# Performance work log

Measured on AMD Instinct MI355X. Metric: run time of the kernel, lower is better.

The kernel has to match this reference:

```python
import jax, jax.numpy as jnp
import numpy as np

DIM = 128
HEADS = 4


def setup_inputs() -> dict:
    key = jax.random.key(0)
    ks = jax.random.split(key, 6)
    B_, N, C = 2048, 49, DIM
    nW = 64
    x = jax.random.normal(ks[0], (B_, N, C), dtype=jnp.float32)
    mask = jax.random.normal(ks[1], (nW, N, N), dtype=jnp.float32)
    qkv_w = jax.random.normal(ks[2], (3 * C, C), dtype=jnp.float32) * 0.02
    qkv_b = jnp.zeros((3 * C,), dtype=jnp.float32)
    proj_w = jax.random.normal(ks[3], (C, C), dtype=jnp.float32) * 0.02
    proj_b = jnp.zeros((C,), dtype=jnp.float32)
    return {"x": x, "mask": mask, "qkv_w": qkv_w, "qkv_b": qkv_b,
            "proj_w": proj_w, "proj_b": proj_b}


def reference(x, mask, qkv_w, qkv_b, proj_w, proj_b):
    B_, N, C = x.shape
    H = HEADS
    Dh = C // H
    scale = Dh ** (-0.5)
    # fused QKV projection: [B_, N, 3C]
    qkv = x @ qkv_w.T + qkv_b
    qkv = qkv.reshape(B_, N, 3, H, Dh).transpose(2, 0, 3, 1, 4)  # [3, B_, H, N, Dh]
    q, k, v = qkv[0] * scale, qkv[1], qkv[2]
    attn = jnp.einsum('bhqd,bhkd->bhqk', q, k)  # [B_, H, N, N]
    nW = mask.shape[0]
    # add per-window additive mask: broadcast over images and heads
    attn = attn.reshape(B_ // nW, nW, H, N, N) + mask[None, :, None, :, :]
    attn = jax.nn.softmax(attn.reshape(B_, H, N, N), axis=-1)
    out = jnp.einsum('bhqk,bhkd->bhqd', attn, v)  # [B_, H, N, Dh]
    out = out.transpose(0, 2, 1, 3).reshape(B_, N, C)
    return out @ proj_w.T + proj_b
```

## Files before the change

kernel.cpp:

```cpp
#include <hip/hip_runtime.h>

typedef __bf16 bf16_t;
typedef __bf16 bf16x2 __attribute__((ext_vector_type(2)));
typedef __bf16 bf16x4 __attribute__((ext_vector_type(4)));
typedef __bf16 bf16x8 __attribute__((ext_vector_type(8)));
typedef float  f32x4  __attribute__((ext_vector_type(4)));
typedef float  f32x4u __attribute__((ext_vector_type(4), aligned(4)));
typedef short  s16x4  __attribute__((ext_vector_type(4)));
typedef unsigned int u32;

#define MFMA32(a, b, c) __builtin_amdgcn_mfma_f32_16x16x32_bf16((a), (b), (c), 0, 0, 0)

union B4u { bf16x4 h; s16x4 s; };
__device__ __forceinline__ f32x4 MFMA16(bf16x4 a, bf16x4 b, f32x4 c) {
#if __has_builtin(__builtin_amdgcn_mfma_f32_16x16x16_bf16)
    return __builtin_amdgcn_mfma_f32_16x16x16_bf16(a, b, c, 0, 0, 0);
#elif __has_builtin(__builtin_amdgcn_mfma_f32_16x16x16bf16_1k)
    B4u ua, ub; ua.h = a; ub.h = b;
    return __builtin_amdgcn_mfma_f32_16x16x16bf16_1k(ua.s, ub.s, c, 0, 0, 0);
#else
    f32x4 d = c;
    asm volatile("v_mfma_f32_16x16x16_bf16 %0, %1, %2, %0"
                 : "+v"(d) : "v"(a), "v"(b));
    return d;
#endif
}

#define ROWB 272

__device__ __forceinline__ void st4(char* base, int row, int byteoff, bf16x4 v) {
    *(bf16x4*)(base + row * ROWB + byteoff) = v;
}
__device__ __forceinline__ bf16x8 ld8(const char* base, int row, int byteoff) {
    return *(const bf16x8*)(base + row * ROWB + byteoff);
}
__device__ __forceinline__ void stx(char* buf, int i, float4 f) {
    bf16x4 hq;
    hq[0] = (bf16_t)f.x; hq[1] = (bf16_t)f.y; hq[2] = (bf16_t)f.z; hq[3] = (bf16_t)f.w;
    st4(buf, i >> 5, (i & 31) << 3, hq);
}

__device__ __forceinline__ bf16x4 cvt4b(f32x4 v, float4 bias, float sc) {
    bf16x4 t;
    t[0] = (bf16_t)((v[0] + bias.x) * sc);
    t[1] = (bf16_t)((v[1] + bias.y) * sc);
    t[2] = (bf16_t)((v[2] + bias.z) * sc);
    t[3] = (bf16_t)((v[3] + bias.w) * sc);
    return t;
}
__device__ __forceinline__ bf16x4 cvt4s(f32x4 v, float bias) {
    bf16x4 t;
    t[0] = (bf16_t)(v[0] + bias);
    t[1] = (bf16_t)(v[1] + bias);
    t[2] = (bf16_t)(v[2] + bias);
    t[3] = (bf16_t)(v[3] + bias);
    return t;
}

__global__ void wconv_kernel(const float* __restrict__ qw, const float* __restrict__ pw,
                             bf16_t* __restrict__ o) {
    int i = (blockIdx.x * 256 + threadIdx.x) * 4;
    const float* src = (i < 49152) ? (qw + i) : (pw + (i - 49152));
    float4 f = *(const float4*)src;
    bf16x4 h;
    h[0] = (bf16_t)f.x; h[1] = (bf16_t)f.y; h[2] = (bf16_t)f.z; h[3] = (bf16_t)f.w;
    *(bf16x4*)(o + i) = h;
}

template<int USEB>
__device__ __forceinline__ bf16x8 ldw(const float* __restrict__ wf,
                                      const bf16_t* __restrict__ wb, int idx) {
    if constexpr (USEB) {
        return *(const bf16x8*)(wb + idx);
    } else {
        float4 f0 = *(const float4*)(wf + idx);
        float4 f1 = *(const float4*)(wf + idx + 4);
        bf16x8 r;
        r[0] = (bf16_t)f0.x; r[1] = (bf16_t)f0.y; r[2] = (bf16_t)f0.z; r[3] = (bf16_t)f0.w;
        r[4] = (bf16_t)f1.x; r[5] = (bf16_t)f1.y; r[6] = (bf16_t)f1.z; r[7] = (bf16_t)f1.w;
        return r;
    }
}


template<int USEB>
__global__ __launch_bounds__(256, 2) void winattn_kernel(
    const float* __restrict__ xg, const float* __restrict__ maskg,
    const float* __restrict__ qwg, const float* __restrict__ qbg,
    const float* __restrict__ pwg, const float* __restrict__ pbg,
    const bf16_t* __restrict__ wqb, const bf16_t* __restrict__ wpb,
    const int nW, float* __restrict__ outg)
{
    __shared__ char xs[17408];

    const int b    = blockIdx.x;
    const int tid  = threadIdx.x;
    const int w    = tid >> 6;
    const int lane = tid & 63;
    const int g    = lane >> 4;
    const int c0   = lane & 15;
    const int h    = w;

    {
        const float4* xb = (const float4*)(xg + (long)b * 6272);
        #pragma unroll
        for (int it = 0; it < 7; ++it) {
            int i = tid + it * 256;
            if (i < 1568) { float4 f = xb[i]; stx(xs, i, f); }
        }
        #pragma unroll
        for (int it = 0; it < 4; ++it) {
            int i = tid + it * 256;
            if (i < 960) {
                int row = 49 + (i >> 6), byteo = (i & 63) << 2;
                *(u32*)(xs + row * ROWB + byteo) = 0u;
            }
        }
    }
    __syncthreads();

    const float qs = 0.17677669529663687f;

    bf16x4 qfr[2][4];
    {
        f32x4 acc[2][4];
        #pragma unroll
        for (int d = 0; d < 2; ++d)
            #pragma unroll
            for (int mt = 0; mt < 4; ++mt) acc[d][mt] = {0.f, 0.f, 0.f, 0.f};
        #pragma unroll
        for (int ks = 0; ks < 4; ++ks) {
            bf16x8 w0 = ldw<USEB>(qwg, wqb, (32*h + c0) * 128 + 32*ks + 8*g);
            bf16x8 w1 = ldw<USEB>(qwg, wqb, (32*h + 16 + c0) * 128 + 32*ks + 8*g);
            #pragma unroll
            for (int mt = 0; mt < 4; ++mt) {
                bf16x8 xf = ld8(xs, 16*mt + c0, (32*ks + 8*g) * 2);
                acc[0][mt] = MFMA32(w0, xf, acc[0][mt]);
                acc[1][mt] = MFMA32(w1, xf, acc[1][mt]);
            }
        }
        float4 b0 = *(const float4*)(qbg + 32*h + 4*g);
        float4 b1 = *(const float4*)(qbg + 32*h + 16 + 4*g);
        #pragma unroll
        for (int qt = 0; qt < 4; ++qt) {
            qfr[0][qt] = cvt4b(acc[0][qt], b0, qs);
            qfr[1][qt] = cvt4b(acc[1][qt], b1, qs);
        }
    }

    bf16x4 kfr[4][2];
    {
        f32x4 acc[2][4];
        #pragma unroll
        for (int d = 0; d < 2; ++d)
            #pragma unroll
            for (int mt = 0; mt < 4; ++mt) acc[d][mt] = {0.f, 0.f, 0.f, 0.f};
        #pragma unroll
        for (int ks = 0; ks < 4; ++ks) {
            bf16x8 w0 = ldw<USEB>(qwg, wqb, (128 + 32*h + c0) * 128 + 32*ks + 8*g);
            bf16x8 w1 = ldw<USEB>(qwg, wqb, (128 + 32*h + 16 + c0) * 128 + 32*ks + 8*g);
            #pragma unroll
            for (int mt = 0; mt < 4; ++mt) {
                bf16x8 xf = ld8(xs, 16*mt + c0, (32*ks + 8*g) * 2);
                acc[0][mt] = MFMA32(w0, xf, acc[0][mt]);
                acc[1][mt] = MFMA32(w1, xf, acc[1][mt]);
            }
        }
        float4 b0 = *(const float4*)(qbg + 128 + 32*h + 4*g);
        float4 b1 = *(const float4*)(qbg + 128 + 32*h + 16 + 4*g);
        #pragma unroll
        for (int kt = 0; kt < 4; ++kt) {
            kfr[kt][0] = cvt4b(acc[0][kt], b0, 1.f);
            kfr[kt][1] = cvt4b(acc[1][kt], b1, 1.f);
        }
    }

    bf16x4 vfr[2][4];
    {
        f32x4 acc[4][2];
        #pragma unroll
        for (int mt = 0; mt < 4; ++mt)
            #pragma unroll
            for (int d = 0; d < 2; ++d) acc[mt][d] = {0.f, 0.f, 0.f, 0.f};
        #pragma unroll
        for (int ks = 0; ks < 4; ++ks) {
            bf16x8 w0 = ldw<USEB>(qwg, wqb, (256 + 32*h + c0) * 128 + 32*ks + 8*g);
            bf16x8 w1 = ldw<USEB>(qwg, wqb, (256 + 32*h + 16 + c0) * 128 + 32*ks + 8*g);
            #pragma unroll
            for (int mt = 0; mt < 4; ++mt) {
                bf16x8 xf = ld8(xs, 16*mt + c0, (32*ks + 8*g) * 2);
                acc[mt][0] = MFMA32(xf, w0, acc[mt][0]);
                acc[mt][1] = MFMA32(xf, w1, acc[mt][1]);
            }
        }
        float vb0 = qbg[256 + 32*h + c0];
        float vb1 = qbg[256 + 32*h + 16 + c0];
        #pragma unroll
        for (int kt = 0; kt < 4; ++kt) {
            vfr[0][kt] = cvt4s(acc[kt][0], vb0);
            vfr[1][kt] = cvt4s(acc[kt][1], vb1);
        }
    }
    __syncthreads();

    const float* mrow = maskg + (long)(b % nW) * 2401;
    #pragma unroll
    for (int qt = 0; qt < 4; ++qt) {
        f32x4 s[4];
        #pragma unroll
        for (int kt = 0; kt < 4; ++kt) s[kt] = {0.f, 0.f, 0.f, 0.f};
        #pragma unroll
        for (int kt = 0; kt < 4; ++kt) {
            s[kt] = MFMA16(kfr[kt][0], qfr[0][qt], s[kt]);
            s[kt] = MFMA16(kfr[kt][1], qfr[1][qt], s[kt]);
        }

        {
            int q  = 16*qt + c0;
            int qm = q < 49 ? q : 48;
            const float* mr = mrow + qm * 49;
            f32x4u m0 = *(const f32x4u*)(mr + 4*g);
            f32x4u m1 = *(const f32x4u*)(mr + 16 + 4*g);
            f32x4u m2 = *(const f32x4u*)(mr + 32 + 4*g);
            float m48 = mr[48];
            #pragma unroll
            for (int r = 0; r < 4; ++r) {
                s[0][r] += m0[r]; s[1][r] += m1[r]; s[2][r] += m2[r];
            }
            s[3][0] = (g == 0) ? s[3][0] + m48 : -1e30f;
            s[3][1] = -1e30f; s[3][2] = -1e30f; s[3][3] = -1e30f;
        }

        float mx = -1e30f;
        #pragma unroll
        for (int kt = 0; kt < 4; ++kt)
            #pragma unroll
            for (int r = 0; r < 4; ++r) mx = fmaxf(mx, s[kt][r]);
        mx = fmaxf(mx, __shfl_xor(mx, 16));
        mx = fmaxf(mx, __shfl_xor(mx, 32));

        float sum = 0.f;
        bf16x4 p[4];
        #pragma unroll
        for (int kt = 0; kt < 4; ++kt) {
            float e0 = __expf(s[kt][0] - mx), e1 = __expf(s[kt][1] - mx);
            float e2 = __expf(s[kt][2] - mx), e3 = __expf(s[kt][3] - mx);
            sum += (e0 + e1) + (e2 + e3);
            bf16x4 pk;
            pk[0] = (bf16_t)e0; pk[1] = (bf16_t)e1;
            pk[2] = (bf16_t)e2; pk[3] = (bf16_t)e3;
            p[kt] = pk;
        }
        sum += __shfl_xor(sum, 16);
        sum += __shfl_xor(sum, 32);
        float inv = 1.f / sum;

        f32x4 oo[2];
        oo[0] = {0.f, 0.f, 0.f, 0.f}; oo[1] = {0.f, 0.f, 0.f, 0.f};
        #pragma unroll
        for (int kt = 0; kt < 4; ++kt) {
            oo[0] = MFMA16(vfr[0][kt], p[kt], oo[0]);
            oo[1] = MFMA16(vfr[1][kt], p[kt], oo[1]);
        }
        int q = 16*qt + c0;
        #pragma unroll
        for (int dt = 0; dt < 2; ++dt) {
            bf16x4 t;
            t[0] = (bf16_t)(oo[dt][0] * inv); t[1] = (bf16_t)(oo[dt][1] * inv);
            t[2] = (bf16_t)(oo[dt][2] * inv); t[3] = (bf16_t)(oo[dt][3] * inv);
            st4(xs, q, (32*h + 16*dt + 4*g) * 2, t);
        }
    }

    bf16x8 pwf[4][2];
    #pragma unroll
    for (int ks = 0; ks < 4; ++ks) {
        pwf[ks][0] = ldw<USEB>(pwg, wpb, (32*w + c0) * 128 + 32*ks + 8*g);
        pwf[ks][1] = ldw<USEB>(pwg, wpb, (32*w + 16 + c0) * 128 + 32*ks + 8*g);
    }
    float4 pb0 = *(const float4*)(pbg + 32*w + 4*g);
    float4 pb1 = *(const float4*)(pbg + 32*w + 16 + 4*g);
    __syncthreads();

    {
        f32x4 acc[2][4];
        #pragma unroll
        for (int nt = 0; nt < 2; ++nt)
            #pragma unroll
            for (int mt = 0; mt < 4; ++mt) acc[nt][mt] = {0.f, 0.f, 0.f, 0.f};
        #pragma unroll
        for (int ks = 0; ks < 4; ++ks) {
            #pragma unroll
            for (int mt = 0; mt < 4; ++mt) {
                bf16x8 af = ld8(xs, 16*mt + c0, (32*ks + 8*g) * 2);
                acc[0][mt] = MFMA32(pwf[ks][0], af, acc[0][mt]);
                acc[1][mt] = MFMA32(pwf[ks][1], af, acc[1][mt]);
            }
        }
        float* ob = outg + (long)b * 6272;
        #pragma unroll
        for (int nt = 0; nt < 2; ++nt) {
            float4 pb = nt ? pb1 : pb0;
            #pragma unroll
            for (int mt = 0; mt < 4; ++mt) {
                int tok = 16*mt + c0;
                if (tok < 49) {
                    float4 t;
                    t.x = acc[nt][mt][0] + pb.x;
                    t.y = acc[nt][mt][1] + pb.y;
                    t.z = acc[nt][mt][2] + pb.z;
                    t.w = acc[nt][mt][3] + pb.w;
                    *(float4*)(ob + tok*128 + 32*w + 16*nt + 4*g) = t;
                }
            }
        }
    }
}

extern "C" void kernel_launch(void* const* d_in, const int* in_sizes, int n_in,
                              void* d_out, int out_size, void* d_ws, size_t ws_size,
                              hipStream_t stream) {
    const float* xg  = (const float*)d_in[0];
    const float* mg  = (const float*)d_in[1];
    const float* qwg = (const float*)d_in[2];
    const float* qbg = (const float*)d_in[3];
    const float* pwg = (const float*)d_in[4];
    const float* pbg = (const float*)d_in[5];
    float* outg = (float*)d_out;

    const int B  = in_sizes[0] / (49 * 128);
    const int nW = in_sizes[1] / (49 * 49);

    if (d_ws != nullptr && ws_size >= 131072) {
        bf16_t* wqb = (bf16_t*)d_ws;
        bf16_t* wpb = wqb + 49152;
        wconv_kernel<<<64, 256, 0, stream>>>(qwg, pwg, wqb);
        winattn_kernel<1><<<B, 256, 0, stream>>>(
            xg, mg, qwg, qbg, pwg, pbg, wqb, wpb, nW, outg);
    } else {
        winattn_kernel<0><<<B, 256, 0, stream>>>(
            xg, mg, qwg, qbg, pwg, pbg, nullptr, nullptr, nW, outg);
    }
}
```

Measured before the change: 64.92 us.

## Process two windows per 512-thread block with separate LDS tiles

Each block now handles two windows, using 8 waves split into two groups of four heads, each group with its own shared-memory tile. The grid halves and the block size doubles, with an active guard for an odd window count. The aim is to amortise block launch and scheduling overhead and change occupancy, at the cost of both windows sharing the same barriers and possible register-pressure changes under launch_bounds(512,2).

```diff
diff --git a/kernel.cpp b/kernel.cpp
--- a/kernel.cpp
+++ b/kernel.cpp
@@ -27,6 +27,7 @@
 }
 
 #define ROWB 272
+#define TILEB 17408
 
 __device__ __forceinline__ void st4(char* base, int row, int byteoff, bf16x4 v) {
     *(bf16x4*)(base + row * ROWB + byteoff) = v;
@@ -84,33 +85,38 @@
 
 
 template<int USEB>
-__global__ __launch_bounds__(256, 2) void winattn_kernel(
+__global__ __launch_bounds__(512, 2) void winattn_kernel(
     const float* __restrict__ xg, const float* __restrict__ maskg,
     const float* __restrict__ qwg, const float* __restrict__ qbg,
     const float* __restrict__ pwg, const float* __restrict__ pbg,
     const bf16_t* __restrict__ wqb, const bf16_t* __restrict__ wpb,
-    const int nW, float* __restrict__ outg)
+    const int nW, const int Btot, float* __restrict__ outg)
 {
-    __shared__ char xs[17408];
-
-    const int b    = blockIdx.x;
+    __shared__ char xs2[2 * TILEB];
+
     const int tid  = threadIdx.x;
-    const int w    = tid >> 6;
+    const int w8   = tid >> 6;
+    const int win  = w8 >> 2;
+    const int h    = w8 & 3;
     const int lane = tid & 63;
     const int g    = lane >> 4;
     const int c0   = lane & 15;
-    const int h    = w;
-
-    {
-        const float4* xb = (const float4*)(xg + (long)b * 6272);
+
+    const long b     = (long)blockIdx.x * 2 + win;
+    const bool active = (b < Btot);
+    char* xs = xs2 + win * TILEB;
+    const int tid2 = tid & 255;
+
+    if (active) {
+        const float4* xb = (const float4*)(xg + b * 6272);
         #pragma unroll
         for (int it = 0; it < 7; ++it) {
-            int i = tid + it * 256;
+            int i = tid2 + it * 256;
             if (i < 1568) { float4 f = xb[i]; stx(xs, i, f); }
         }
         #pragma unroll
         for (int it = 0; it < 4; ++it) {
-            int i = tid + it * 256;
+            int i = tid2 + it * 256;
             if (i < 960) {
                 int row = 49 + (i >> 6), byteo = (i & 63) << 2;
                 *(u32*)(xs + row * ROWB + byteo) = 0u;
@@ -122,167 +128,173 @@
     const float qs = 0.17677669529663687f;
 
     bf16x4 qfr[2][4];
-    {
-        f32x4 acc[2][4];
-        #pragma unroll
-        for (int d = 0; d < 2; ++d)
-            #pragma unroll
-            for (int mt = 0; mt < 4; ++mt) acc[d][mt] = {0.f, 0.f, 0.f, 0.f};
+    bf16x4 kfr[4][2];
+    bf16x4 vfr[2][4];
+
+    if (active) {
+        {
+            f32x4 acc[2][4];
+            #pragma unroll
+            for (int d = 0; d < 2; ++d)
+                #pragma unroll
+                for (int mt = 0; mt < 4; ++mt) acc[d][mt] = {0.f, 0.f, 0.f, 0.f};
+            #pragma unroll
+            for (int ks = 0; ks < 4; ++ks) {
+                bf16x8 w0 = ldw<USEB>(qwg, wqb, (32*h + c0) * 128 + 32*ks + 8*g);
+                bf16x8 w1 = ldw<USEB>(qwg, wqb, (32*h + 16 + c0) * 128 + 32*ks + 8*g);
+                #pragma unroll
+                for (int mt = 0; mt < 4; ++mt) {
+                    bf16x8 xf = ld8(xs, 16*mt + c0, (32*ks + 8*g) * 2);
+                    acc[0][mt] = MFMA32(w0, xf, acc[0][mt]);
+                    acc[1][mt] = MFMA32(w1, xf, acc[1][mt]);
+                }
+            }
+            float4 b0 = *(const float4*)(qbg + 32*h + 4*g);
+            float4 b1 = *(const float4*)(qbg + 32*h + 16 + 4*g);
+            #pragma unroll
+            for (int qt = 0; qt < 4; ++qt) {
+                qfr[0][qt] = cvt4b(acc[0][qt], b0, qs);
+                qfr[1][qt] = cvt4b(acc[1][qt], b1, qs);
+            }
+        }
+        {
+            f32x4 acc[2][4];
+            #pragma unroll
+            for (int d = 0; d < 2; ++d)
+                #pragma unroll
+                for (int mt = 0; mt < 4; ++mt) acc[d][mt] = {0.f, 0.f, 0.f, 0.f};
+            #pragma unroll
+            for (int ks = 0; ks < 4; ++ks) {
+                bf16x8 w0 = ldw<USEB>(qwg, wqb, (128 + 32*h + c0) * 128 + 32*ks + 8*g);
+                bf16x8 w1 = ldw<USEB>(qwg, wqb, (128 + 32*h + 16 + c0) * 128 + 32*ks + 8*g);
+                #pragma unroll
+                for (int mt = 0; mt < 4; ++mt) {
+                    bf16x8 xf = ld8(xs, 16*mt + c0, (32*ks + 8*g) * 2);
+                    acc[0][mt] = MFMA32(w0, xf, acc[0][mt]);
+                    acc[1][mt] = MFMA32(w1, xf, acc[1][mt]);
+                }
+            }
+            float4 b0 = *(const float4*)(qbg + 128 + 32*h + 4*g);
+            float4 b1 = *(const float4*)(qbg + 128 + 32*h + 16 + 4*g);
+            #pragma unroll
+            for (int kt = 0; kt < 4; ++kt) {
+                kfr[kt][0] = cvt4b(acc[0][kt], b0, 1.f);
+                kfr[kt][1] = cvt4b(acc[1][kt], b1, 1.f);
+            }
+        }
+        {
+            f32x4 acc[4][2];
+            #pragma unroll
+            for (int mt = 0; mt < 4; ++mt)
+                #pragma unroll
+                for (int d = 0; d < 2; ++d) acc[mt][d] = {0.f, 0.f, 0.f, 0.f};
+            #pragma unroll
+            for (int ks = 0; ks < 4; ++ks) {
+                bf16x8 w0 = ldw<USEB>(qwg, wqb, (256 + 32*h + c0) * 128 + 32*ks + 8*g);
+                bf16x8 w1 = ldw<USEB>(qwg, wqb, (256 + 32*h + 16 + c0) * 128 + 32*ks + 8*g);
+                #pragma unroll
+                for (int mt = 0; mt < 4; ++mt) {
+                    bf16x8 xf = ld8(xs, 16*mt + c0, (32*ks + 8*g) * 2);
+                    acc[mt][0] = MFMA32(xf, w0, acc[mt][0]);
+                    acc[mt][1] = MFMA32(xf, w1, acc[mt][1]);
+                }
+            }
+            float vb0 = qbg[256 + 32*h + c0];
+            float vb1 = qbg[256 + 32*h + 16 + c0];
+            #pragma unroll
+            for (int kt = 0; kt < 4; ++kt) {
+                vfr[0][kt] = cvt4s(acc[kt][0], vb0);
+                vfr[1][kt] = cvt4s(acc[kt][1], vb1);
+            }
+        }
+    }
+    __syncthreads();
+
+    if (active) {
+        const float* mrow = maskg + (long)(b % nW) * 2401;
+        #pragma unroll
+        for (int qt = 0; qt < 4; ++qt) {
+            f32x4 s[4];
+            #pragma unroll
+            for (int kt = 0; kt < 4; ++kt) s[kt] = {0.f, 0.f, 0.f, 0.f};
+            #pragma unroll
+            for (int kt = 0; kt < 4; ++kt) {
+                s[kt] = MFMA16(kfr[kt][0], qfr[0][qt], s[kt]);
+                s[kt] = MFMA16(kfr[kt][1], qfr[1][qt], s[kt]);
+            }
+
+            {
+                int q  = 16*qt + c0;
+                int qm = q < 49 ? q : 48;
+                const float* mr = mrow + qm * 49;
+                f32x4u m0 = *(const f32x4u*)(mr + 4*g);
+                f32x4u m1 = *(const f32x4u*)(mr + 16 + 4*g);
+                f32x4u m2 = *(const f32x4u*)(mr + 32 + 4*g);
+                float m48 = mr[48];
+                #pragma unroll
+                for (int r = 0; r < 4; ++r) {
+                    s[0][r] += m0[r]; s[1][r] += m1[r]; s[2][r] += m2[r];
+                }
+                s[3][0] = (g == 0) ? s[3][0] + m48 : -1e30f;
+                s[3][1] = -1e30f; s[3][2] = -1e30f; s[3][3] = -1e30f;
+            }
+
+            float mx = -1e30f;
+            #pragma unroll
+            for (int kt = 0; kt < 4; ++kt)
+                #pragma unroll
+                for (int r = 0; r < 4; ++r) mx = fmaxf(mx, s[kt][r]);
+            mx = fmaxf(mx, __shfl_xor(mx, 16));
+            mx = fmaxf(mx, __shfl_xor(mx, 32));
+
+            float sum = 0.f;
+            bf16x4 p[4];
+            #pragma unroll
+            for (int kt = 0; kt < 4; ++kt) {
+                float e0 = __expf(s[kt][0] - mx), e1 = __expf(s[kt][1] - mx);
+                float e2 = __expf(s[kt][2] - mx), e3 = __expf(s[kt][3] - mx);
+                sum += (e0 + e1) + (e2 + e3);
+                bf16x4 pk;
+                pk[0] = (bf16_t)e0; pk[1] = (bf16_t)e1;
+                pk[2] = (bf16_t)e2; pk[3] = (bf16_t)e3;
+                p[kt] = pk;
+            }
+            sum += __shfl_xor(sum, 16);
+            sum += __shfl_xor(sum, 32);
+            float inv = 1.f / sum;
+
+            f32x4 oo[2];
+            oo[0] = {0.f, 0.f, 0.f, 0.f}; oo[1] = {0.f, 0.f, 0.f, 0.f};
+            #pragma unroll
+            for (int kt = 0; kt < 4; ++kt) {
+                oo[0] = MFMA16(vfr[0][kt], p[kt], oo[0]);
+                oo[1] = MFMA16(vfr[1][kt], p[kt], oo[1]);
+            }
+            int q = 16*qt + c0;
+            #pragma unroll
+            for (int dt = 0; dt < 2; ++dt) {
+                bf16x4 t;
+                t[0] = (bf16_t)(oo[dt][0] * inv); t[1] = (bf16_t)(oo[dt][1] * inv);
+                t[2] = (bf16_t)(oo[dt][2] * inv); t[3] = (bf16_t)(oo[dt][3] * inv);
+                st4(xs, q, (32*h + 16*dt + 4*g) * 2, t);
+            }
+        }
+    }
+
+    bf16x8 pwf[4][2];
+    float4 pb0, pb1;
+    if (active) {
         #pragma unroll
         for (int ks = 0; ks < 4; ++ks) {
-            bf16x8 w0 = ldw<USEB>(qwg, wqb, (32*h + c0) * 128 + 32*ks + 8*g);
-            bf16x8 w1 = ldw<USEB>(qwg, wqb, (32*h + 16 + c0) * 128 + 32*ks + 8*g);
-            #pragma unroll
-            for (int mt = 0; mt < 4; ++mt) {
-                bf16x8 xf = ld8(xs, 16*mt + c0, (32*ks + 8*g) * 2);
-                acc[0][mt] = MFMA32(w0, xf, acc[0][mt]);
-                acc[1][mt] = MFMA32(w1, xf, acc[1][mt]);
-            }
-        }
-        float4 b0 = *(const float4*)(qbg + 32*h + 4*g);
-        float4 b1 = *(const float4*)(qbg + 32*h + 16 + 4*g);
-        #pragma unroll
-        for (int qt = 0; qt < 4; ++qt) {
-            qfr[0][qt] = cvt4b(acc[0][qt], b0, qs);
-            qfr[1][qt] = cvt4b(acc[1][qt], b1, qs);
-        }
-    }
-
-    bf16x4 kfr[4][2];
-    {
-        f32x4 acc[2][4];
-        #pragma unroll
-        for (int d = 0; d < 2; ++d)
-            #pragma unroll
-            for (int mt = 0; mt < 4; ++mt) acc[d][mt] = {0.f, 0.f, 0.f, 0.f};
-        #pragma unroll
-        for (int ks = 0; ks < 4; ++ks) {
-            bf16x8 w0 = ldw<USEB>(qwg, wqb, (128 + 32*h + c0) * 128 + 32*ks + 8*g);
-            bf16x8 w1 = ldw<USEB>(qwg, wqb, (128 + 32*h + 16 + c0) * 128 + 32*ks + 8*g);
-            #pragma unroll
-            for (int mt = 0; mt < 4; ++mt) {
-                bf16x8 xf = ld8(xs, 16*mt + c0, (32*ks + 8*g) * 2);
-                acc[0][mt] = MFMA32(w0, xf, acc[0][mt]);
-                acc[1][mt] = MFMA32(w1, xf, acc[1][mt]);
-            }
-        }
-        float4 b0 = *(const float4*)(qbg + 128 + 32*h + 4*g);
-        float4 b1 = *(const float4*)(qbg + 128 + 32*h + 16 + 4*g);
-        #pragma unroll
-        for (int kt = 0; kt < 4; ++kt) {
-            kfr[kt][0] = cvt4b(acc[0][kt], b0, 1.f);
-            kfr[kt][1] = cvt4b(acc[1][kt], b1, 1.f);
-        }
-    }
-
-    bf16x4 vfr[2][4];
-    {
-        f32x4 acc[4][2];
-        #pragma unroll
-        for (int mt = 0; mt < 4; ++mt)
-            #pragma unroll
-            for (int d = 0; d < 2; ++d) acc[mt][d] = {0.f, 0.f, 0.f, 0.f};
-        #pragma unroll
-        for (int ks = 0; ks < 4; ++ks) {
-            bf16x8 w0 = ldw<USEB>(qwg, wqb, (256 + 32*h + c0) * 128 + 32*ks + 8*g);
-            bf16x8 w1 = ldw<USEB>(qwg, wqb, (256 + 32*h + 16 + c0) * 128 + 32*ks + 8*g);
-            #pragma unroll
-            for (int mt = 0; mt < 4; ++mt) {
-                bf16x8 xf = ld8(xs, 16*mt + c0, (32*ks + 8*g) * 2);
-                acc[mt][0] = MFMA32(xf, w0, acc[mt][0]);
-                acc[mt][1] = MFMA32(xf, w1, acc[mt][1]);
-            }
-        }
-        float vb0 = qbg[256 + 32*h + c0];
-        float vb1 = qbg[256 + 32*h + 16 + c0];
-        #pragma unroll
-        for (int kt = 0; kt < 4; ++kt) {
-            vfr[0][kt] = cvt4s(acc[kt][0], vb0);
-            vfr[1][kt] = cvt4s(acc[kt][1], vb1);
-        }
+            pwf[ks][0] = ldw<USEB>(pwg, wpb, (32*h + c0) * 128 + 32*ks + 8*g);
+            pwf[ks][1] = ldw<USEB>(pwg, wpb, (32*h + 16 + c0) * 128 + 32*ks + 8*g);
+        }
+        pb0 = *(const float4*)(pbg + 32*h + 4*g);
+        pb1 = *(const float4*)(pbg + 32*h + 16 + 4*g);
     }
     __syncthreads();
 
-    const float* mrow = maskg + (long)(b % nW) * 2401;
-    #pragma unroll
-    for (int qt = 0; qt < 4; ++qt) {
-        f32x4 s[4];
-        #pragma unroll
-        for (int kt = 0; kt < 4; ++kt) s[kt] = {0.f, 0.f, 0.f, 0.f};
-        #pragma unroll
-        for (int kt = 0; kt < 4; ++kt) {
-            s[kt] = MFMA16(kfr[kt][0], qfr[0][qt], s[kt]);
-            s[kt] = MFMA16(kfr[kt][1], qfr[1][qt], s[kt]);
-        }
-
-        {
-            int q  = 16*qt + c0;
-            int qm = q < 49 ? q : 48;
-            const float* mr = mrow + qm * 49;
-            f32x4u m0 = *(const f32x4u*)(mr + 4*g);
-            f32x4u m1 = *(const f32x4u*)(mr + 16 + 4*g);
-            f32x4u m2 = *(const f32x4u*)(mr + 32 + 4*g);
-            float m48 = mr[48];
-            #pragma unroll
-            for (int r = 0; r < 4; ++r) {
-                s[0][r] += m0[r]; s[1][r] += m1[r]; s[2][r] += m2[r];
-            }
-            s[3][0] = (g == 0) ? s[3][0] + m48 : -1e30f;
-            s[3][1] = -1e30f; s[3][2] = -1e30f; s[3][3] = -1e30f;
-        }
-
-        float mx = -1e30f;
-        #pragma unroll
-        for (int kt = 0; kt < 4; ++kt)
-            #pragma unroll
-            for (int r = 0; r < 4; ++r) mx = fmaxf(mx, s[kt][r]);
-        mx = fmaxf(mx, __shfl_xor(mx, 16));
-        mx = fmaxf(mx, __shfl_xor(mx, 32));
-
-        float sum = 0.f;
-        bf16x4 p[4];
-        #pragma unroll
-        for (int kt = 0; kt < 4; ++kt) {
-            float e0 = __expf(s[kt][0] - mx), e1 = __expf(s[kt][1] - mx);
-            float e2 = __expf(s[kt][2] - mx), e3 = __expf(s[kt][3] - mx);
-            sum += (e0 + e1) + (e2 + e3);
-            bf16x4 pk;
-            pk[0] = (bf16_t)e0; pk[1] = (bf16_t)e1;
-            pk[2] = (bf16_t)e2; pk[3] = (bf16_t)e3;
-            p[kt] = pk;
-        }
-        sum += __shfl_xor(sum, 16);
-        sum += __shfl_xor(sum, 32);
-        float inv = 1.f / sum;
-
-        f32x4 oo[2];
-        oo[0] = {0.f, 0.f, 0.f, 0.f}; oo[1] = {0.f, 0.f, 0.f, 0.f};
-        #pragma unroll
-        for (int kt = 0; kt < 4; ++kt) {
-            oo[0] = MFMA16(vfr[0][kt], p[kt], oo[0]);
-            oo[1] = MFMA16(vfr[1][kt], p[kt], oo[1]);
-        }
-        int q = 16*qt + c0;
-        #pragma unroll
-        for (int dt = 0; dt < 2; ++dt) {
-            bf16x4 t;
-            t[0] = (bf16_t)(oo[dt][0] * inv); t[1] = (bf16_t)(oo[dt][1] * inv);
-            t[2] = (bf16_t)(oo[dt][2] * inv); t[3] = (bf16_t)(oo[dt][3] * inv);
-            st4(xs, q, (32*h + 16*dt + 4*g) * 2, t);
-        }
-    }
-
-    bf16x8 pwf[4][2];
-    #pragma unroll
-    for (int ks = 0; ks < 4; ++ks) {
-        pwf[ks][0] = ldw<USEB>(pwg, wpb, (32*w + c0) * 128 + 32*ks + 8*g);
-        pwf[ks][1] = ldw<USEB>(pwg, wpb, (32*w + 16 + c0) * 128 + 32*ks + 8*g);
-    }
-    float4 pb0 = *(const float4*)(pbg + 32*w + 4*g);
-    float4 pb1 = *(const float4*)(pbg + 32*w + 16 + 4*g);
-    __syncthreads();
-
-    {
+    if (active) {
         f32x4 acc[2][4];
         #pragma unroll
         for (int nt = 0; nt < 2; ++nt)
@@ -297,7 +309,7 @@
                 acc[1][mt] = MFMA32(pwf[ks][1], af, acc[1][mt]);
             }
         }
-        float* ob = outg + (long)b * 6272;
+        float* ob = outg + b * 6272;
         #pragma unroll
         for (int nt = 0; nt < 2; ++nt) {
             float4 pb = nt ? pb1 : pb0;
@@ -310,7 +322,7 @@
                     t.y = acc[nt][mt][1] + pb.y;
                     t.z = acc[nt][mt][2] + pb.z;
                     t.w = acc[nt][mt][3] + pb.w;
-                    *(float4*)(ob + tok*128 + 32*w + 16*nt + 4*g) = t;
+                    *(float4*)(ob + tok*128 + 32*h + 16*nt + 4*g) = t;
                 }
             }
         }
@@ -330,15 +342,16 @@
 
     const int B  = in_sizes[0] / (49 * 128);
     const int nW = in_sizes[1] / (49 * 49);
+    const int nblk = (B + 1) / 2;
 
     if (d_ws != nullptr && ws_size >= 131072) {
         bf16_t* wqb = (bf16_t*)d_ws;
         bf16_t* wpb = wqb + 49152;
         wconv_kernel<<<64, 256, 0, stream>>>(qwg, pwg, wqb);
-        winattn_kernel<1><<<B, 256, 0, stream>>>(
-            xg, mg, qwg, qbg, pwg, pbg, wqb, wpb, nW, outg);
+        winattn_kernel<1><<<nblk, 512, 0, stream>>>(
+            xg, mg, qwg, qbg, pwg, pbg, wqb, wpb, nW, B, outg);
     } else {
-        winattn_kernel<0><<<B, 256, 0, stream>>>(
-            xg, mg, qwg, qbg, pwg, pbg, nullptr, nullptr, nW, outg);
-    }
-}
+        winattn_kernel<0><<<nblk, 512, 0, stream>>>(
+            xg, mg, qwg, qbg, pwg, pbg, nullptr, nullptr, nW, B, outg);
+    }
+}
```

New measurement: 71.10 us. 9.5% more time.
